# Optimization experiments

Hardware: AMD Instinct MI355X
Metric: run time of the kernel (lower is better)

The kernel has to match this reference:

```python
import jax, jax.numpy as jnp
import numpy as np

K_BINS = 8192
HIDDEN = 2048
SQRT2 = 1.4142135623730951
LEAKY_SLOPE = 0.01
TMIN = 1e-10


def setup_inputs() -> dict:
    key = jax.random.key(0)
    k0, k1, k2 = jax.random.split(key, 3)
    D = 2 * K_BINS  # mu length so that cat([mu, t]) has 2K+1 features
    # positive mu keeps mu ** (gamma - 1/(1-gamma)) (a fractional power) finite
    mu = jax.random.uniform(k0, (D,), jnp.float32, 0.1, 1.0)
    t = jnp.array([0.5], jnp.float32)
    gamma = jnp.array([0.5], jnp.float32)  # 1/(1-gamma) = 2 -> integral exponent
    W1 = jax.random.normal(k1, (D + 1, HIDDEN), jnp.float32) * (1.0 / np.sqrt(D + 1))
    b1 = jnp.zeros((HIDDEN,), jnp.float32)
    W2 = jax.random.normal(k2, (HIDDEN, D), jnp.float32) * (1.0 / np.sqrt(HIDDEN))
    b2 = jnp.zeros((D,), jnp.float32)
    return {"mu": mu, "t": t, "gamma": gamma, "W1": W1, "b1": b1,
            "W2": W2, "b2": b2, "K": K_BINS}


def reference(mu, t, gamma, W1, b1, W2, b2, K):
    g = gamma[0]
    # --- NN(cat([mu, t])) -> (mu_epsilon, ln_sigma_epsilon), each [K] ---
    inp = jnp.concatenate([mu, t])                      # [2K+1]
    h = jax.nn.leaky_relu(inp @ W1 + b1, LEAKY_SLOPE)   # [hidden]
    out = h @ W2 + b2                                   # [2K]
    mu_eps, ln_sig = out[:K], out[K:]
    # --- mu_x / sigma_x (t < tmin branch folded in via where) ---
    p_mu = g - 1.0 / (1.0 - g)
    p_eps = 1.0 / (1.0 - g)
    mu_x_nn = jnp.power(mu[:K], p_mu) * jnp.power(mu_eps, p_eps)
    sigma_x_nn = jnp.power(1.0 - g, -0.5) * jnp.exp(0.5 * ln_sig)
    use_nn = t[0] >= TMIN
    mu_x = jnp.where(use_nn, mu_x_nn, jnp.zeros_like(mu_eps))     # [K]
    sigma_x = jnp.where(use_nn, sigma_x_nn, jnp.ones_like(mu_eps))  # [K]
    # --- vectorized discretised CDF differences over the (D_out, K) grid ---
    kk = jnp.arange(K, dtype=jnp.float32)
    kl = 2.0 * (kk - 1.0) / (K - 1.0)   # left bin edges  [K]
    kr = 2.0 * kk / (K - 1.0)           # right bin edges [K]

    def cdf(x):  # x: [K] edges -> G: [D_out, K]
        z = (x[None, :] - mu_x[:, None]) / (sigma_x[:, None] * SQRT2)
        F = 0.5 * (1.0 + jax.lax.erf(z))
        return jnp.where(x[None, :] <= -1.0, 0.0,
                         jnp.where(x[None, :] >= 1.0, 1.0, F))

    return cdf(kr) - cdf(kl)  # [K, K] per-bin probabilities
```

## Files before the change

### kernel.cpp

```cpp
#include <hip/hip_runtime.h>
#include <math.h>

#define KBINS 8192
#define DDIM  16384
#define HID   2048
#define LASTROW 16384

#define C1 8
#define NCH1 2048
#define NCH2 256

static constexpr float SQRT2_F  = 1.4142135623730951f;
static constexpr float INVSQ2PI = 0.3989422804014327f;

__device__ __forceinline__ float fast_erff(float x) {
    float ax = fabsf(x);
    float t  = 1.0f / fmaf(0.3275911f, ax, 1.0f);
    float p  = t * (0.254829592f +
               t * (-0.284496736f +
               t * (1.421413741f +
               t * (-1.453152027f +
               t * 1.061405429f))));
    float r = 1.0f - p * __expf(-ax * ax);
    return copysignf(r, x);
}

__global__ void __launch_bounds__(256)
mv1_partial(const float* __restrict__ mu, const float* __restrict__ W1,
            float* __restrict__ part1) {
    __shared__ float a_s[C1];
    int r0 = blockIdx.x * C1;
    if (threadIdx.x < C1) a_s[threadIdx.x] = mu[r0 + threadIdx.x];
    __syncthreads();
    int c0 = threadIdx.x * 4;
    const float* wp = W1 + (size_t)r0 * HID;
    float4 acc0 = {0.f, 0.f, 0.f, 0.f};
    float4 acc1 = {0.f, 0.f, 0.f, 0.f};
#pragma unroll
    for (int k = 0; k < C1; ++k) {
        float a = a_s[k];
        const float4 w0 = *reinterpret_cast<const float4*>(wp + (size_t)k * HID + c0);
        const float4 w1 = *reinterpret_cast<const float4*>(wp + (size_t)k * HID + c0 + 1024);
        acc0.x += a * w0.x; acc0.y += a * w0.y; acc0.z += a * w0.z; acc0.w += a * w0.w;
        acc1.x += a * w1.x; acc1.y += a * w1.y; acc1.z += a * w1.z; acc1.w += a * w1.w;
    }
    float* pp = part1 + (size_t)blockIdx.x * HID;
    *reinterpret_cast<float4*>(pp + c0)        = acc0;
    *reinterpret_cast<float4*>(pp + c0 + 1024) = acc1;
}

__global__ void __launch_bounds__(256)
mv2h(const float* __restrict__ part1, const float* __restrict__ b1,
     const float* __restrict__ W1, const float* __restrict__ t,
     const float* __restrict__ W2, float* __restrict__ part2) {
    __shared__ float red[32][8];
    __shared__ float hs[8];
    const int tid   = threadIdx.x;
    const int r0    = blockIdx.y * 8;
    const int cbase = blockIdx.x * 4096;
    {
        int cl  = tid & 7;
        int sub = tid >> 3;
        float s = 0.f;
        const float* p = part1 + r0 + cl;
#pragma unroll 8
        for (int m = 0; m < 64; ++m)
            s += p[(size_t)(sub + (m << 5)) * HID];
        red[sub][cl] = s;
    }
    __syncthreads();
    if (tid < 8) {
        int r = r0 + tid;
        float v = b1[r] + t[0] * W1[(size_t)LASTROW * HID + r];
#pragma unroll
        for (int q = 0; q < 32; ++q) v += red[q][tid];
        hs[tid] = (v >= 0.f) ? v : 0.01f * v;
    }
    __syncthreads();
    int c0 = cbase + tid * 4;
    float4 acc[4];
#pragma unroll
    for (int q = 0; q < 4; ++q) acc[q] = {0.f, 0.f, 0.f, 0.f};
    const float* wp = W2 + (size_t)r0 * DDIM + c0;
#pragma unroll 2
    for (int k = 0; k < 8; ++k) {
        float a = hs[k];
        const float* wr = wp + (size_t)k * DDIM;
#pragma unroll
        for (int q = 0; q < 4; ++q) {
            const float4 w = *reinterpret_cast<const float4*>(wr + q * 1024);
            acc[q].x += a * w.x; acc[q].y += a * w.y;
            acc[q].z += a * w.z; acc[q].w += a * w.w;
        }
    }
    float* pp = part2 + (size_t)blockIdx.y * DDIM + c0;
#pragma unroll
    for (int q = 0; q < 4; ++q)
        *reinterpret_cast<float4*>(pp + q * 1024) = acc[q];
}

__global__ void __launch_bounds__(256)
cdf_fused(const float* __restrict__ part2, const float* __restrict__ b2,
          const float* __restrict__ mu, const float* __restrict__ t,
          const float* __restrict__ gamma, float* __restrict__ out) {
    __shared__ float red[32][8];
    __shared__ float sv[8];
    __shared__ float sA[4], sB[4], sCf[4], sEr[4];
    const int tid = threadIdx.x;
    const int i0  = blockIdx.x * 4;
    {
        int col = tid & 7;
        int sub = tid >> 3;
        int gc  = (col < 4) ? (i0 + col) : (KBINS + i0 + col - 4);
        float s = 0.f;
        const float* p = part2 + gc;
#pragma unroll 8
        for (int m = 0; m < 8; ++m)
            s += p[(size_t)(sub + (m << 5)) * DDIM];
        red[sub][col] = s;
    }
    __syncthreads();
    if (tid < 8) {
        int gc = (tid < 4) ? (i0 + tid) : (KBINS + i0 + tid - 4);
        float v = b2[gc];
#pragma unroll
        for (int q = 0; q < 32; ++q) v += red[q][tid];
        sv[tid] = v;
    }
    __syncthreads();
    if (tid < 4) {
        float s0 = sv[tid];
        float s1 = sv[tid + 4];
        float g  = gamma[0];
        float pe = 1.0f / (1.0f - g);
        float pm = g - pe;
        bool use_nn = (t[0] >= 1e-10f);
        float mval = use_nn ? powf(mu[i0 + tid], pm) * powf(s0, pe) : 0.0f;
        float invs = use_nn ? powf(1.0f - g, 0.5f) * expf(-0.5f * s1) : 1.0f;
        const float sc = 2.0f / 8191.0f;
        float A = sc * invs;
        sA[tid]  = A;
        sB[tid]  = (-1.0f / 8191.0f - mval) * invs;
        sCf[tid] = INVSQ2PI * A;
        float z = (8190.0f / 8191.0f - mval) * invs * (1.0f / SQRT2_F);
        sEr[tid] = 0.5f * (1.0f - fast_erff(z));
    }
    __syncthreads();
    for (int rr = 0; rr < 4; ++rr) {
        float A    = sA[rr];
        float B    = sB[rr];
        float coef = sCf[rr];
        float er   = sEr[rr];
        float* orow = out + (size_t)(i0 + rr) * KBINS;
#pragma unroll
        for (int it = 0; it < 8; ++it) {
            int j0 = it * 1024 + tid * 4;
            float4 r;
            if (j0 < 4096) {
                float u0 = fmaf((float)j0, A, B);
                float u1 = u0 + A;
                float u2 = u1 + A;
                float u3 = u2 + A;
                r.x = coef * __expf(-0.5f * u0 * u0);
                r.y = coef * __expf(-0.5f * u1 * u1);
                r.z = coef * __expf(-0.5f * u2 * u2);
                r.w = coef * __expf(-0.5f * u3 * u3);
            } else if (j0 == 4096) {
                r.x = er;
                r.y = r.z = r.w = 0.f;
            } else {
                r.x = r.y = r.z = r.w = 0.f;
            }
            *reinterpret_cast<float4*>(orow + j0) = r;
        }
    }
}

extern "C" void kernel_launch(void* const* d_in, const int* in_sizes, int n_in,
                              void* d_out, int out_size, void* d_ws, size_t ws_size,
                              hipStream_t stream) {
    const float* mu    = (const float*)d_in[0];
    const float* t     = (const float*)d_in[1];
    const float* gamma = (const float*)d_in[2];
    const float* W1    = (const float*)d_in[3];
    const float* b1    = (const float*)d_in[4];
    const float* W2    = (const float*)d_in[5];
    const float* b2    = (const float*)d_in[6];
    float* out = (float*)d_out;

    float* ws    = (float*)d_ws;
    float* part1 = ws;
    float* part2 = part1 + (size_t)NCH1 * HID;

    mv1_partial<<<dim3(NCH1),    dim3(256), 0, stream>>>(mu, W1, part1);
    mv2h       <<<dim3(4, NCH2), dim3(256), 0, stream>>>(part1, b1, W1, t, W2, part2);
    cdf_fused  <<<dim3(2048),    dim3(256), 0, stream>>>(part2, b2, mu, t, gamma, out);
}
```

Before: 163.6 us.

## Split hidden reduction into separate kernel and widen W2 row chunks

The fused reduce+matvec kernel recomputed the part1 reduction in each of the four column blocks, so the 16MB partial buffer was read four times. A dedicated h_reduce kernel now computes the hidden activations once, and a new mv2_partial kernel processes 16 rows per block, halving the part2 partial buffer and the CDF kernel's reduction reads. This adds a kernel launch and a small global round-trip for h.

```diff
diff --git a/kernel.cpp b/kernel.cpp
--- a/kernel.cpp
+++ b/kernel.cpp
@@ -8,7 +8,8 @@
 
 #define C1 8
 #define NCH1 2048
-#define NCH2 256
+#define C2 16
+#define NCH2 128
 
 static constexpr float SQRT2_F  = 1.4142135623730951f;
 static constexpr float INVSQ2PI = 0.3989422804014327f;
@@ -50,53 +51,52 @@
 }
 
 __global__ void __launch_bounds__(256)
-mv2h(const float* __restrict__ part1, const float* __restrict__ b1,
-     const float* __restrict__ W1, const float* __restrict__ t,
-     const float* __restrict__ W2, float* __restrict__ part2) {
-    __shared__ float red[32][8];
-    __shared__ float hs[8];
-    const int tid   = threadIdx.x;
-    const int r0    = blockIdx.y * 8;
-    const int cbase = blockIdx.x * 4096;
-    {
-        int cl  = tid & 7;
-        int sub = tid >> 3;
-        float s = 0.f;
-        const float* p = part1 + r0 + cl;
+h_reduce(const float* __restrict__ part1, const float* __restrict__ b1,
+         const float* __restrict__ W1, const float* __restrict__ t,
+         float* __restrict__ h) {
+    __shared__ float red[32][9];
+    int col_l = threadIdx.x & 7;
+    int sub   = threadIdx.x >> 3;
+    int c0    = blockIdx.x * 8;
+    float s = 0.f;
+    const float* p = part1 + c0 + col_l;
 #pragma unroll 8
-        for (int m = 0; m < 64; ++m)
-            s += p[(size_t)(sub + (m << 5)) * HID];
-        red[sub][cl] = s;
-    }
-    __syncthreads();
-    if (tid < 8) {
-        int r = r0 + tid;
-        float v = b1[r] + t[0] * W1[(size_t)LASTROW * HID + r];
-#pragma unroll
-        for (int q = 0; q < 32; ++q) v += red[q][tid];
-        hs[tid] = (v >= 0.f) ? v : 0.01f * v;
-    }
-    __syncthreads();
-    int c0 = cbase + tid * 4;
-    float4 acc[4];
-#pragma unroll
-    for (int q = 0; q < 4; ++q) acc[q] = {0.f, 0.f, 0.f, 0.f};
-    const float* wp = W2 + (size_t)r0 * DDIM + c0;
-#pragma unroll 2
-    for (int k = 0; k < 8; ++k) {
-        float a = hs[k];
-        const float* wr = wp + (size_t)k * DDIM;
-#pragma unroll
-        for (int q = 0; q < 4; ++q) {
-            const float4 w = *reinterpret_cast<const float4*>(wr + q * 1024);
-            acc[q].x += a * w.x; acc[q].y += a * w.y;
-            acc[q].z += a * w.z; acc[q].w += a * w.w;
-        }
-    }
-    float* pp = part2 + (size_t)blockIdx.y * DDIM + c0;
-#pragma unroll
-    for (int q = 0; q < 4; ++q)
-        *reinterpret_cast<float4*>(pp + q * 1024) = acc[q];
+    for (int m = 0; m < 64; ++m)
+        s += p[(size_t)(sub + (m << 5)) * HID];
+    red[sub][col_l] = s;
+    __syncthreads();
+    if (threadIdx.x < 8) {
+        int c = c0 + threadIdx.x;
+        float v = b1[c] + t[0] * W1[(size_t)LASTROW * HID + c];
+#pragma unroll
+        for (int q = 0; q < 32; ++q) v += red[q][threadIdx.x];
+        h[c] = (v >= 0.f) ? v : 0.01f * v;
+    }
+}
+
+__global__ void __launch_bounds__(256)
+mv2_partial(const float* __restrict__ h, const float* __restrict__ W2,
+            float* __restrict__ part2) {
+    __shared__ float hs[C2];
+    int r0    = blockIdx.y * C2;
+    int cbase = blockIdx.x * 1024;
+    if (threadIdx.x < C2) hs[threadIdx.x] = h[r0 + threadIdx.x];
+    __syncthreads();
+    int c0 = cbase + threadIdx.x * 4;
+    const float* wp = W2 + (size_t)r0 * DDIM;
+    float4 acc0 = {0.f, 0.f, 0.f, 0.f};
+    float4 acc1 = {0.f, 0.f, 0.f, 0.f};
+#pragma unroll
+    for (int k = 0; k < C2; k += 2) {
+        float a0 = hs[k];
+        float a1 = hs[k + 1];
+        const float4 w0 = *reinterpret_cast<const float4*>(wp + (size_t)k * DDIM + c0);
+        const float4 w1 = *reinterpret_cast<const float4*>(wp + (size_t)(k + 1) * DDIM + c0);
+        acc0.x += a0 * w0.x; acc0.y += a0 * w0.y; acc0.z += a0 * w0.z; acc0.w += a0 * w0.w;
+        acc1.x += a1 * w1.x; acc1.y += a1 * w1.y; acc1.z += a1 * w1.z; acc1.w += a1 * w1.w;
+    }
+    float4 acc = {acc0.x + acc1.x, acc0.y + acc1.y, acc0.z + acc1.z, acc0.w + acc1.w};
+    *reinterpret_cast<float4*>(part2 + (size_t)blockIdx.y * DDIM + c0) = acc;
 }
 
 __global__ void __launch_bounds__(256)
@@ -114,8 +114,8 @@
         int gc  = (col < 4) ? (i0 + col) : (KBINS + i0 + col - 4);
         float s = 0.f;
         const float* p = part2 + gc;
-#pragma unroll 8
-        for (int m = 0; m < 8; ++m)
+#pragma unroll
+        for (int m = 0; m < 4; ++m)
             s += p[(size_t)(sub + (m << 5)) * DDIM];
         red[sub][col] = s;
     }
@@ -190,9 +190,11 @@
 
     float* ws    = (float*)d_ws;
     float* part1 = ws;
-    float* part2 = part1 + (size_t)NCH1 * HID;
-
-    mv1_partial<<<dim3(NCH1),    dim3(256), 0, stream>>>(mu, W1, part1);
-    mv2h       <<<dim3(4, NCH2), dim3(256), 0, stream>>>(part1, b1, W1, t, W2, part2);
-    cdf_fused  <<<dim3(2048),    dim3(256), 0, stream>>>(part2, b2, mu, t, gamma, out);
-}
+    float* h     = part1 + (size_t)NCH1 * HID;
+    float* part2 = h + HID;
+
+    mv1_partial<<<dim3(NCH1),      dim3(256), 0, stream>>>(mu, W1, part1);
+    h_reduce   <<<dim3(256),       dim3(256), 0, stream>>>(part1, b1, W1, t, h);
+    mv2_partial<<<dim3(16, NCH2),  dim3(256), 0, stream>>>(h, W2, part2);
+    cdf_fused  <<<dim3(2048),      dim3(256), 0, stream>>>(part2, b2, mu, t, gamma, out);
+}
```

Measured after the change: 143.6 us. 1.14x faster.
